# Kernel tuning notes

Hardware: AMD Instinct MI355X
Metric: run time of the kernel (lower is better)

The kernel has to match this reference:

```python
import jax, jax.numpy as jnp
import numpy as np

B, S, E = 4, 2048, 2048
NH, NKV, HD = 16, 4, 128  # num_heads, num_kv_heads, head_dim
GROUP = NH // NKV


def setup_inputs() -> dict:
    key = jax.random.key(0)
    ks = jax.random.split(key, 6)
    sc = 0.02
    return {
        "hidden_states": jax.random.normal(ks[0], (B, S, E), dtype=jnp.float32),
        "q_w": jax.random.normal(ks[1], (E, NH * HD), dtype=jnp.float32) * sc,
        "k_w": jax.random.normal(ks[2], (E, NKV * HD), dtype=jnp.float32) * sc,
        "v_w": jax.random.normal(ks[3], (E, NKV * HD), dtype=jnp.float32) * sc,
        "out_w": jax.random.normal(ks[4], (NH * HD, E), dtype=jnp.float32) * sc,
        "out_b": jnp.zeros((E,), dtype=jnp.float32),
    }


def reference(hidden_states, q_w, k_w, v_w, out_w, out_b):
    x = hidden_states
    # projections (no bias on q/k/v, bias on out_proj)
    q = (x @ q_w).reshape(B, S, NH, HD).transpose(0, 2, 1, 3)    # [B,NH,S,HD]
    k = (x @ k_w).reshape(B, S, NKV, HD).transpose(0, 2, 1, 3)   # [B,NKV,S,HD]
    v = (x @ v_w).reshape(B, S, NKV, HD).transpose(0, 2, 1, 3)   # [B,NKV,S,HD]

    # GQA: each kv head serves GROUP consecutive query heads (matches loop order)
    k_exp = jnp.repeat(k, GROUP, axis=1)  # [B,NH,S,HD]
    v_exp = jnp.repeat(v, GROUP, axis=1)

    # GPT-Neo: fp32 attention, NO 1/sqrt(d) scaling
    qf = q.astype(jnp.float32)
    kf = k_exp.astype(jnp.float32)
    scores = jnp.einsum("bhqd,bhkd->bhqk", qf, kf)  # [B,NH,S,S]

    causal = jnp.tril(jnp.ones((S, S), dtype=bool))[None, None]
    mask_value = jnp.finfo(scores.dtype).min
    scores = jnp.where(causal, scores, mask_value)

    attn = jax.nn.softmax(scores, axis=-1).astype(v.dtype)
    ctx = jnp.einsum("bhqk,bhkd->bhqd", attn, v_exp)  # [B,NH,S,HD]

    out = ctx.transpose(0, 2, 1, 3).reshape(B, S, NH * HD)
    return out @ out_w + out_b
```

## Files before the change

kernel.cpp:

```cpp
#include <hip/hip_runtime.h>

typedef unsigned short u16;
typedef unsigned int   u32;
typedef __attribute__((ext_vector_type(8))) _Float16 f16x8;
typedef __attribute__((ext_vector_type(2))) __fp16   fp16x2;
typedef __attribute__((ext_vector_type(4))) float    f32x4;

#define LOG2E 1.44269504088896340f

__device__ __forceinline__ u16 f2h(float x) {
  union { _Float16 h; u16 u; } c;
  c.h = (_Float16)x;
  return c.u;
}
__device__ __forceinline__ u32 pk2(float a, float b) {
  union { fp16x2 h; u32 u; } c;
  c.h = __builtin_amdgcn_cvt_pkrtz(a, b);
  return c.u;
}
__device__ __forceinline__ void swap32(u32& a, u32& b) {
  asm volatile("v_permlane32_swap_b32 %0, %1" : "+v"(a), "+v"(b));
}
__device__ __forceinline__ void swap16(u32& a, u32& b) {
  asm volatile("v_permlane16_swap_b32 %0, %1" : "+v"(a), "+v"(b));
}
__device__ __forceinline__ void gload16(const u16* g, u16* l) {
  __builtin_amdgcn_global_load_lds(
      (const __attribute__((address_space(1))) void*)g,
      (__attribute__((address_space(3))) void*)l, 16, 0, 0);
}
__device__ __forceinline__ f32x4 MFMA(f16x8 a, f16x8 b, f32x4 c) {
  return __builtin_amdgcn_mfma_f32_16x16x32_f16(a, b, c, 0, 0, 0);
}

__global__ void conv_f16(const float4* __restrict__ src, u16* __restrict__ d, int n4) {
  int i = blockIdx.x * 256 + threadIdx.x;
  if (i >= n4) return;
  float4 v = src[i];
  union { u16 u[4]; uint2 q; } H;
  H.u[0] = f2h(v.x); H.u[1] = f2h(v.y); H.u[2] = f2h(v.z); H.u[3] = f2h(v.w);
  *(uint2*)&d[(size_t)i * 4] = H.q;
}

__global__ void transpose_f16(const float* __restrict__ src, int K, int N,
                              u16* __restrict__ d, int rowOff) {
  __shared__ float t[32][33];
  int n0 = blockIdx.x * 32, k0 = blockIdx.y * 32;
  int tx = threadIdx.x, ty = threadIdx.y;
#pragma unroll
  for (int i = 0; i < 4; ++i)
    t[ty + 8 * i][tx] = src[(size_t)(k0 + ty + 8 * i) * N + n0 + tx];
  __syncthreads();
#pragma unroll
  for (int i = 0; i < 4; ++i) {
    int n = n0 + ty + 8 * i, k = k0 + tx;
    d[(size_t)(rowOff + n) * 2048 + k] = f2h(t[tx][ty + 8 * i]);
  }
}

__global__ __launch_bounds__(512) void gemm_qkv(
    const u16* __restrict__ A, const u16* __restrict__ B,
    u16* __restrict__ Qf, u16* __restrict__ Kf, u16* __restrict__ VT) {
  const int K = 2048;
  const int NS = K / 32;
  __shared__ u16 As[2][256 * 32];
  __shared__ u16 Bs[2][128 * 32];
  int tid = threadIdx.x;
  int l = tid & 63, w = tid >> 6;
  int lr = l & 15, lg = l >> 4;
  int wr = w >> 1, wc = w & 1;
  int p = blockIdx.x;
  int lidx = (p & 7) * 96 + (p >> 3);
  int bx = lidx % 24, by = lidx / 24;
  int rowA = by * 256, colB = bx * 128;
  int r0 = tid >> 2;
  int ssrc = (((tid & 3) ^ ((r0 >> 1) & 3))) * 8;
  const u16* ga = A + (size_t)(rowA + r0) * K + ssrc;
  const u16* gb = B + (size_t)(colB + r0) * K + ssrc;
  size_t half = (size_t)128 * K;
  f32x4 acc[4][4] = {};
  int swz = (lr >> 1) & 3;

  auto STAGE = [&](int kb, int bi) {
    gload16(ga + kb, &As[bi][tid * 8]);
    gload16(ga + kb + half, &As[bi][4096 + tid * 8]);
    gload16(gb + kb, &Bs[bi][tid * 8]);
  };
  auto COMPUTE = [&](int bi) {
    f16x8 ah[4], bh4[4];
#pragma unroll
    for (int i = 0; i < 4; ++i) {
      ah[i]  = *(const f16x8*)&As[bi][(wr * 64 + i * 16 + lr) * 32 + (lg ^ swz) * 8];
      bh4[i] = *(const f16x8*)&Bs[bi][(wc * 64 + i * 16 + lr) * 32 + (lg ^ swz) * 8];
    }
    __builtin_amdgcn_s_setprio(1);
#pragma unroll
    for (int i = 0; i < 4; ++i)
#pragma unroll
      for (int j = 0; j < 4; ++j)
        acc[i][j] = MFMA(ah[i], bh4[j], acc[i][j]);
    __builtin_amdgcn_s_setprio(0);
  };

  STAGE(0, 0);
  asm volatile("s_waitcnt vmcnt(0)" ::: "memory");
  __builtin_amdgcn_sched_barrier(0);
  __builtin_amdgcn_s_barrier();
  __builtin_amdgcn_sched_barrier(0);
  for (int t = 0; t < NS; ++t) {
    if (t + 1 < NS) STAGE((t + 1) * 32, (t + 1) & 1);
    COMPUTE(t & 1);
    asm volatile("s_waitcnt vmcnt(0) lgkmcnt(0)" ::: "memory");
    __builtin_amdgcn_sched_barrier(0);
    __builtin_amdgcn_s_barrier();
    __builtin_amdgcn_sched_barrier(0);
  }

#pragma unroll
  for (int i = 0; i < 4; ++i) {
    int row0 = rowA + wr * 64 + i * 16 + lg * 4;
#pragma unroll
    for (int j = 0; j < 4; ++j) {
      int c = colB + wc * 64 + j * 16 + lr;
      f32x4 v = acc[i][j];
      if (c < 2048) {
#pragma unroll
        for (int r = 0; r < 4; ++r)
          Qf[(size_t)(row0 + r) * 2048 + c] = f2h(v[r]);
      } else if (c < 2560) {
        int ck = c - 2048;
#pragma unroll
        for (int r = 0; r < 4; ++r)
          Kf[(size_t)(row0 + r) * 512 + ck] = f2h(v[r]);
      } else {
        int cv = c - 2560, kvh = cv >> 7, d = cv & 127;
        int b = row0 >> 11, t2 = row0 & 2047;
        union { u16 u[4]; uint2 q; } P;
#pragma unroll
        for (int r = 0; r < 4; ++r) P.u[r] = f2h(v[r]);
        *(uint2*)&VT[((size_t)(b * 4 + kvh) * 128 + d) * 2048 + t2] = P.q;
      }
    }
  }
}

__global__ __launch_bounds__(512) void gemm_out(
    const u16* __restrict__ A, const u16* __restrict__ B,
    float* __restrict__ Out, const float* __restrict__ bias) {
  const int K = 2048;
  const int NS = K / 32;
  __shared__ u16 As[2][256 * 32];
  __shared__ u16 Bs[2][128 * 32];
  int tid = threadIdx.x;
  int l = tid & 63, w = tid >> 6;
  int lr = l & 15, lg = l >> 4;
  int wr = w >> 1, wc = w & 1;
  int p = blockIdx.x;
  int lidx = (p & 7) * 64 + (p >> 3);
  int bx = lidx & 15, by = lidx >> 4;
  int rowA = by * 256, colB = bx * 128;
  int r0 = tid >> 2;
  int ssrc = (((tid & 3) ^ ((r0 >> 1) & 3))) * 8;
  const u16* ga = A + (size_t)(rowA + r0) * K + ssrc;
  const u16* gb = B + (size_t)(colB + r0) * K + ssrc;
  size_t half = (size_t)128 * K;
  f32x4 acc[4][4] = {};
  int swz = (lr >> 1) & 3;

  auto STAGE = [&](int kb, int bi) {
    gload16(ga + kb, &As[bi][tid * 8]);
    gload16(ga + kb + half, &As[bi][4096 + tid * 8]);
    gload16(gb + kb, &Bs[bi][tid * 8]);
  };
  auto COMPUTE = [&](int bi) {
    f16x8 ah[4], bh4[4];
#pragma unroll
    for (int i = 0; i < 4; ++i) {
      ah[i]  = *(const f16x8*)&As[bi][(wr * 64 + i * 16 + lr) * 32 + (lg ^ swz) * 8];
      bh4[i] = *(const f16x8*)&Bs[bi][(wc * 64 + i * 16 + lr) * 32 + (lg ^ swz) * 8];
    }
    __builtin_amdgcn_s_setprio(1);
#pragma unroll
    for (int i = 0; i < 4; ++i)
#pragma unroll
      for (int j = 0; j < 4; ++j)
        acc[i][j] = MFMA(ah[i], bh4[j], acc[i][j]);
    __builtin_amdgcn_s_setprio(0);
  };

  STAGE(0, 0);
  asm volatile("s_waitcnt vmcnt(0)" ::: "memory");
  __builtin_amdgcn_sched_barrier(0);
  __builtin_amdgcn_s_barrier();
  __builtin_amdgcn_sched_barrier(0);
  for (int t = 0; t < NS; ++t) {
    if (t + 1 < NS) STAGE((t + 1) * 32, (t + 1) & 1);
    COMPUTE(t & 1);
    asm volatile("s_waitcnt vmcnt(0) lgkmcnt(0)" ::: "memory");
    __builtin_amdgcn_sched_barrier(0);
    __builtin_amdgcn_s_barrier();
    __builtin_amdgcn_sched_barrier(0);
  }

#pragma unroll
  for (int i = 0; i < 4; ++i) {
    int row0 = rowA + wr * 64 + i * 16 + lg * 4;
#pragma unroll
    for (int j = 0; j < 4; ++j) {
      int c = colB + wc * 64 + j * 16 + lr;
      float bb = bias[c];
#pragma unroll
      for (int r = 0; r < 4; ++r)
        Out[(size_t)(row0 + r) * 2048 + c] = acc[i][j][r] + bb;
    }
  }
}

__global__ __launch_bounds__(512) void attn_kernel(
    const u16* __restrict__ Qf, const u16* __restrict__ Kf,
    const u16* __restrict__ VT, u16* __restrict__ Ch) {
  __shared__ u16 Ks[2][64 * 128];
  __shared__ u16 Vs[2][128 * 64];

  int tid = threadIdx.x;
  int w = tid >> 6, l = tid & 63;
  int lr = l & 15, lg = l >> 4;

  int p = blockIdx.x;
  int bid = (p & 7) * 64 + (p >> 3);
  int pair = bid & 7;
  int hg = (bid >> 3) & 3;
  int kvh = (bid >> 5) & 3;
  int b = bid >> 7;
  int h = kvh * 4 + hg;

  const u16* Kb = Kf + (size_t)(b * 2048) * 512 + kvh * 128;
  const u16* Vb = VT + (size_t)((b * 4 + kvh) * 128) * 2048;

  auto STAGE_K = [&](int t, int bufi) {
    int kv0 = t * 64;
#pragma unroll
    for (int pp = 0; pp < 2; ++pp) {
      int o16 = pp * 512 + tid;
      int krow = o16 >> 4;
      int kslot = ((o16 & 15) ^ (krow & 7)) * 8;
      gload16(Kb + (size_t)(kv0 + krow) * 512 + kslot, &Ks[bufi][o16 * 8]);
    }
  };
  auto STAGE_V = [&](int t, int bufi) {
    int kv0 = t * 64;
#pragma unroll
    for (int pp = 0; pp < 2; ++pp) {
      int o16 = pp * 512 + tid;
      int vrow = o16 >> 3;
      int vslot = ((o16 & 7) ^ (vrow & 7)) * 8;
      gload16(Vb + (size_t)vrow * 2048 + kv0 + vslot, &Vs[bufi][o16 * 8]);
    }
  };

  for (int pass = 0; pass < 2; ++pass) {
    int tIdx = pass == 0 ? (15 - pair) : pair;
    int q0 = tIdx * 128;
    int qr0 = q0 + w * 16;
    int nt = q0 / 64 + 2;

    size_t qbase = (size_t)(b * 2048 + qr0 + lr) * 2048 + h * 128 + lg * 8;
    f16x8 qf[4];
#pragma unroll
    for (int d = 0; d < 4; ++d)
      qf[d] = *(const f16x8*)(Qf + qbase + d * 32);

    f32x4 o[8] = {};
    float mrun = -3e38f;
    float lp = 0.f;

    STAGE_K(0, 0);
    STAGE_V(0, 0);
    asm volatile("s_waitcnt vmcnt(0)" ::: "memory");
    __builtin_amdgcn_sched_barrier(0);
    __builtin_amdgcn_s_barrier();
    __builtin_amdgcn_sched_barrier(0);

    int cur = 0;
    for (int t = 0; t < nt; ++t) {
      int kv0 = t * 64;
      bool more = (t + 1 < nt);
      if (more) {
        STAGE_K(t + 1, cur ^ 1);
        STAGE_V(t + 1, cur ^ 1);
      }
      bool compute = (kv0 <= qr0 + 15);

      if (compute) {
        f32x4 s[4] = {};
        __builtin_amdgcn_s_setprio(1);
#pragma unroll
        for (int d = 0; d < 4; ++d) {
#pragma unroll
          for (int n = 0; n < 4; ++n) {
            int row = n * 16 + lr;
            int sl = ((d * 4 + lg) ^ (row & 7)) * 8;
            f16x8 kf = *(const f16x8*)&Ks[cur][row * 128 + sl];
            s[n] = MFMA(kf, qf[d], s[n]);
          }
        }
        __builtin_amdgcn_s_setprio(0);
        if (kv0 + 63 > qr0) {
#pragma unroll
          for (int n = 0; n < 4; ++n)
#pragma unroll
            for (int r = 0; r < 4; ++r)
              if (kv0 + n * 16 + lg * 4 + r > qr0 + lr) s[n][r] = -3e38f;
        }
        float m0 = fmaxf(fmaxf(s[0][0], s[0][1]), fmaxf(s[0][2], s[0][3]));
        float m1 = fmaxf(fmaxf(s[1][0], s[1][1]), fmaxf(s[1][2], s[1][3]));
        float m2 = fmaxf(fmaxf(s[2][0], s[2][1]), fmaxf(s[2][2], s[2][3]));
        float m3 = fmaxf(fmaxf(s[3][0], s[3][1]), fmaxf(s[3][2], s[3][3]));
        float rowmax = fmaxf(fmaxf(m0, m1), fmaxf(m2, m3));
        if (__any(rowmax > mrun + 8.f)) {
          float tm = rowmax;
          tm = fmaxf(tm, __shfl_xor(tm, 16));
          tm = fmaxf(tm, __shfl_xor(tm, 32));
          float mn = fmaxf(mrun, tm);
          float alpha = __builtin_amdgcn_exp2f((mrun - mn) * LOG2E);
          mrun = mn;
          lp *= alpha;
#pragma unroll
          for (int dt = 0; dt < 8; ++dt)
#pragma unroll
            for (int r = 0; r < 4; ++r) o[dt][r] *= alpha;
        }
        float mL = mrun * LOG2E;
        float pv[4][4];
#pragma unroll
        for (int n = 0; n < 4; ++n)
#pragma unroll
          for (int r = 0; r < 4; ++r) {
            pv[n][r] = __builtin_amdgcn_exp2f(fmaf(s[n][r], LOG2E, -mL));
            lp += pv[n][r];
          }
        u32 A0[4], A1[4];
#pragma unroll
        for (int n = 0; n < 4; ++n) {
          A0[n] = pk2(pv[n][0], pv[n][1]);
          A1[n] = pk2(pv[n][2], pv[n][3]);
        }
        swap32(A0[0], A0[2]); swap32(A0[1], A0[3]);
        swap32(A1[0], A1[2]); swap32(A1[1], A1[3]);
        swap16(A0[0], A0[2]); swap16(A0[1], A0[3]);
        swap16(A1[0], A1[2]); swap16(A1[1], A1[3]);
        swap32(A0[0], A0[1]); swap32(A0[2], A0[3]);
        swap32(A1[0], A1[1]); swap32(A1[2], A1[3]);
        union { u32 w4[4]; f16x8 v; } P0, P1;
        P0.w4[0] = A0[0]; P0.w4[1] = A1[0]; P0.w4[2] = A0[2]; P0.w4[3] = A1[2];
        P1.w4[0] = A0[1]; P1.w4[1] = A1[1]; P1.w4[2] = A0[3]; P1.w4[3] = A1[3];
        __builtin_amdgcn_s_setprio(1);
#pragma unroll
        for (int n2 = 0; n2 < 2; ++n2) {
          f16x8 pf = n2 ? P1.v : P0.v;
#pragma unroll
          for (int dt = 0; dt < 8; ++dt) {
            int d = dt * 16 + lr;
            f16x8 vf = *(const f16x8*)&Vs[cur][d * 64 + (((n2 * 4 + lg) ^ (lr & 7)) * 8)];
            o[dt] = MFMA(vf, pf, o[dt]);
          }
        }
        __builtin_amdgcn_s_setprio(0);
      }
      asm volatile("s_waitcnt vmcnt(0) lgkmcnt(0)" ::: "memory");
      __builtin_amdgcn_sched_barrier(0);
      __builtin_amdgcn_s_barrier();
      __builtin_amdgcn_sched_barrier(0);
      cur ^= 1;
    }
    lp += __shfl_xor(lp, 16);
    lp += __shfl_xor(lp, 32);
    float inv = 1.0f / lp;
    size_t orow = (size_t)(b * 2048 + qr0 + lr) * 2048 + h * 128 + lg * 4;
#pragma unroll
    for (int dt = 0; dt < 8; ++dt) {
      uint2 pkt;
      pkt.x = pk2(o[dt][0] * inv, o[dt][1] * inv);
      pkt.y = pk2(o[dt][2] * inv, o[dt][3] * inv);
      *(uint2*)&Ch[orow + dt * 16] = pkt;
    }
  }
}

extern "C" void kernel_launch(void* const* d_in, const int* in_sizes, int n_in,
                              void* d_out, int out_size, void* d_ws, size_t ws_size,
                              hipStream_t stream) {
  const float* X  = (const float*)d_in[0];
  const float* qw = (const float*)d_in[1];
  const float* kw = (const float*)d_in[2];
  const float* vw = (const float*)d_in[3];
  const float* ow = (const float*)d_in[4];
  const float* ob = (const float*)d_in[5];
  float* Out = (float*)d_out;

  char* ws = (char*)d_ws;
  size_t off = 0;
  auto alloc = [&](size_t bytes) -> void* {
    void* p = ws + off;
    off += (bytes + 255) & ~(size_t)255;
    return p;
  };
  const size_t MK = (size_t)8192 * 2048;
  u16* Xf = (u16*)alloc(MK * 2);
  u16* Bt = (u16*)alloc((size_t)3072 * 2048 * 2);
  u16* OW = (u16*)alloc((size_t)2048 * 2048 * 2);
  u16* Qf = (u16*)alloc(MK * 2);
  u16* Kf = (u16*)alloc((size_t)8192 * 512 * 2);
  u16* VT = (u16*)alloc((size_t)8192 * 512 * 2);
  u16* Ch = (u16*)alloc(MK * 2);

  conv_f16<<<dim3(16384), dim3(256), 0, stream>>>((const float4*)X, Xf, (int)(MK / 4));
  dim3 tb(32, 8);
  transpose_f16<<<dim3(64, 64), tb, 0, stream>>>(qw, 2048, 2048, Bt, 0);
  transpose_f16<<<dim3(16, 64), tb, 0, stream>>>(kw, 2048, 512, Bt, 2048);
  transpose_f16<<<dim3(16, 64), tb, 0, stream>>>(vw, 2048, 512, Bt, 2560);
  transpose_f16<<<dim3(64, 64), tb, 0, stream>>>(ow, 2048, 2048, OW, 0);
  gemm_qkv<<<dim3(768), dim3(512), 0, stream>>>(Xf, Bt, Qf, Kf, VT);
  attn_kernel<<<dim3(512), dim3(512), 0, stream>>>(Qf, Kf, VT, Ch);
  gemm_out<<<dim3(512), dim3(512), 0, stream>>>(Ch, OW, Out, ob);
}
```

Measured before the change: 356.8 us.

## Triple-buffer GEMM smem with two-stage-ahead prefetch and split compute phases

Both projection GEMM kernels move from double to triple-buffered LDS, prefetching the K-slice two iterations ahead and waiting with partial vmcnt rather than draining all loads. Each iteration is split into two MFMA halves with a barrier between them, and the global loads are interleaved with the LDS reads so memory latency overlaps compute. The cost is 50% more shared memory per block, which may lower occupancy, plus an extra barrier per iteration.

```diff
diff --git a/kernel.cpp b/kernel.cpp
--- a/kernel.cpp
+++ b/kernel.cpp
@@ -63,8 +63,8 @@
     u16* __restrict__ Qf, u16* __restrict__ Kf, u16* __restrict__ VT) {
   const int K = 2048;
   const int NS = K / 32;
-  __shared__ u16 As[2][256 * 32];
-  __shared__ u16 Bs[2][128 * 32];
+  __shared__ u16 As[3][256 * 32];
+  __shared__ u16 Bs[3][128 * 32];
   int tid = threadIdx.x;
   int l = tid & 63, w = tid >> 6;
   int lr = l & 15, lg = l >> 4;
@@ -80,38 +80,62 @@
   size_t half = (size_t)128 * K;
   f32x4 acc[4][4] = {};
   int swz = (lr >> 1) & 3;
-
-  auto STAGE = [&](int kb, int bi) {
-    gload16(ga + kb, &As[bi][tid * 8]);
-    gload16(ga + kb + half, &As[bi][4096 + tid * 8]);
-    gload16(gb + kb, &Bs[bi][tid * 8]);
-  };
-  auto COMPUTE = [&](int bi) {
-    f16x8 ah[4], bh4[4];
-#pragma unroll
-    for (int i = 0; i < 4; ++i) {
-      ah[i]  = *(const f16x8*)&As[bi][(wr * 64 + i * 16 + lr) * 32 + (lg ^ swz) * 8];
-      bh4[i] = *(const f16x8*)&Bs[bi][(wc * 64 + i * 16 + lr) * 32 + (lg ^ swz) * 8];
-    }
-    __builtin_amdgcn_s_setprio(1);
-#pragma unroll
-    for (int i = 0; i < 4; ++i)
-#pragma unroll
-      for (int j = 0; j < 4; ++j)
-        acc[i][j] = MFMA(ah[i], bh4[j], acc[i][j]);
-    __builtin_amdgcn_s_setprio(0);
-  };
-
-  STAGE(0, 0);
-  asm volatile("s_waitcnt vmcnt(0)" ::: "memory");
+  int aoff = (wr * 64 + lr) * 32 + (lg ^ swz) * 8;
+  int boff = (wc * 64 + lr) * 32 + (lg ^ swz) * 8;
+
+  gload16(ga, &As[0][tid * 8]);
+  gload16(ga + half, &As[0][4096 + tid * 8]);
+  gload16(gb, &Bs[0][tid * 8]);
+  gload16(ga + 32, &As[1][tid * 8]);
+  gload16(ga + 32 + half, &As[1][4096 + tid * 8]);
+  gload16(gb + 32, &Bs[1][tid * 8]);
+  asm volatile("s_waitcnt vmcnt(3)" ::: "memory");
   __builtin_amdgcn_sched_barrier(0);
   __builtin_amdgcn_s_barrier();
   __builtin_amdgcn_sched_barrier(0);
+
   for (int t = 0; t < NS; ++t) {
-    if (t + 1 < NS) STAGE((t + 1) * 32, (t + 1) & 1);
-    COMPUTE(t & 1);
-    asm volatile("s_waitcnt vmcnt(0) lgkmcnt(0)" ::: "memory");
-    __builtin_amdgcn_sched_barrier(0);
+    int cur = t % 3, nxt = (t + 2) % 3;
+    bool pre = (t + 2 < NS);
+    int kb2 = (t + 2) * 32;
+    f16x8 ah[4], bh0, bh1;
+#pragma unroll
+    for (int i = 0; i < 4; ++i)
+      ah[i] = *(const f16x8*)&As[cur][aoff + i * 16 * 32];
+    bh0 = *(const f16x8*)&Bs[cur][boff];
+    bh1 = *(const f16x8*)&Bs[cur][boff + 16 * 32];
+    if (pre) {
+      gload16(ga + kb2, &As[nxt][tid * 8]);
+      gload16(ga + kb2 + half, &As[nxt][4096 + tid * 8]);
+    }
+    asm volatile("s_waitcnt lgkmcnt(0)" ::: "memory");
+    __builtin_amdgcn_sched_barrier(0);
+    __builtin_amdgcn_s_setprio(1);
+#pragma unroll
+    for (int i = 0; i < 4; ++i) {
+      acc[i][0] = MFMA(ah[i], bh0, acc[i][0]);
+      acc[i][1] = MFMA(ah[i], bh1, acc[i][1]);
+    }
+    __builtin_amdgcn_s_setprio(0);
+    __builtin_amdgcn_s_barrier();
+    __builtin_amdgcn_sched_barrier(0);
+    f16x8 bh2 = *(const f16x8*)&Bs[cur][boff + 32 * 32];
+    f16x8 bh3 = *(const f16x8*)&Bs[cur][boff + 48 * 32];
+    if (pre) gload16(gb + kb2, &Bs[nxt][tid * 8]);
+    if (pre) {
+      asm volatile("s_waitcnt vmcnt(3)" ::: "memory");
+    } else {
+      asm volatile("s_waitcnt vmcnt(0)" ::: "memory");
+    }
+    asm volatile("s_waitcnt lgkmcnt(0)" ::: "memory");
+    __builtin_amdgcn_sched_barrier(0);
+    __builtin_amdgcn_s_setprio(1);
+#pragma unroll
+    for (int i = 0; i < 4; ++i) {
+      acc[i][2] = MFMA(ah[i], bh2, acc[i][2]);
+      acc[i][3] = MFMA(ah[i], bh3, acc[i][3]);
+    }
+    __builtin_amdgcn_s_setprio(0);
     __builtin_amdgcn_s_barrier();
     __builtin_amdgcn_sched_barrier(0);
   }
@@ -149,8 +173,8 @@
     float* __restrict__ Out, const float* __restrict__ bias) {
   const int K = 2048;
   const int NS = K / 32;
-  __shared__ u16 As[2][256 * 32];
-  __shared__ u16 Bs[2][128 * 32];
+  __shared__ u16 As[3][256 * 32];
+  __shared__ u16 Bs[3][128 * 32];
   int tid = threadIdx.x;
   int l = tid & 63, w = tid >> 6;
   int lr = l & 15, lg = l >> 4;
@@ -166,38 +190,62 @@
   size_t half = (size_t)128 * K;
   f32x4 acc[4][4] = {};
   int swz = (lr >> 1) & 3;
-
-  auto STAGE = [&](int kb, int bi) {
-    gload16(ga + kb, &As[bi][tid * 8]);
-    gload16(ga + kb + half, &As[bi][4096 + tid * 8]);
-    gload16(gb + kb, &Bs[bi][tid * 8]);
-  };
-  auto COMPUTE = [&](int bi) {
-    f16x8 ah[4], bh4[4];
-#pragma unroll
-    for (int i = 0; i < 4; ++i) {
-      ah[i]  = *(const f16x8*)&As[bi][(wr * 64 + i * 16 + lr) * 32 + (lg ^ swz) * 8];
-      bh4[i] = *(const f16x8*)&Bs[bi][(wc * 64 + i * 16 + lr) * 32 + (lg ^ swz) * 8];
-    }
-    __builtin_amdgcn_s_setprio(1);
-#pragma unroll
-    for (int i = 0; i < 4; ++i)
-#pragma unroll
-      for (int j = 0; j < 4; ++j)
-        acc[i][j] = MFMA(ah[i], bh4[j], acc[i][j]);
-    __builtin_amdgcn_s_setprio(0);
-  };
-
-  STAGE(0, 0);
-  asm volatile("s_waitcnt vmcnt(0)" ::: "memory");
+  int aoff = (wr * 64 + lr) * 32 + (lg ^ swz) * 8;
+  int boff = (wc * 64 + lr) * 32 + (lg ^ swz) * 8;
+
+  gload16(ga, &As[0][tid * 8]);
+  gload16(ga + half, &As[0][4096 + tid * 8]);
+  gload16(gb, &Bs[0][tid * 8]);
+  gload16(ga + 32, &As[1][tid * 8]);
+  gload16(ga + 32 + half, &As[1][4096 + tid * 8]);
+  gload16(gb + 32, &Bs[1][tid * 8]);
+  asm volatile("s_waitcnt vmcnt(3)" ::: "memory");
   __builtin_amdgcn_sched_barrier(0);
   __builtin_amdgcn_s_barrier();
   __builtin_amdgcn_sched_barrier(0);
+
   for (int t = 0; t < NS; ++t) {
-    if (t + 1 < NS) STAGE((t + 1) * 32, (t + 1) & 1);
-    COMPUTE(t & 1);
-    asm volatile("s_waitcnt vmcnt(0) lgkmcnt(0)" ::: "memory");
-    __builtin_amdgcn_sched_barrier(0);
+    int cur = t % 3, nxt = (t + 2) % 3;
+    bool pre = (t + 2 < NS);
+    int kb2 = (t + 2) * 32;
+    f16x8 ah[4], bh0, bh1;
+#pragma unroll
+    for (int i = 0; i < 4; ++i)
+      ah[i] = *(const f16x8*)&As[cur][aoff + i * 16 * 32];
+    bh0 = *(const f16x8*)&Bs[cur][boff];
+    bh1 = *(const f16x8*)&Bs[cur][boff + 16 * 32];
+    if (pre) {
+      gload16(ga + kb2, &As[nxt][tid * 8]);
+      gload16(ga + kb2 + half, &As[nxt][4096 + tid * 8]);
+    }
+    asm volatile("s_waitcnt lgkmcnt(0)" ::: "memory");
+    __builtin_amdgcn_sched_barrier(0);
+    __builtin_amdgcn_s_setprio(1);
+#pragma unroll
+    for (int i = 0; i < 4; ++i) {
+      acc[i][0] = MFMA(ah[i], bh0, acc[i][0]);
+      acc[i][1] = MFMA(ah[i], bh1, acc[i][1]);
+    }
+    __builtin_amdgcn_s_setprio(0);
+    __builtin_amdgcn_s_barrier();
+    __builtin_amdgcn_sched_barrier(0);
+    f16x8 bh2 = *(const f16x8*)&Bs[cur][boff + 32 * 32];
+    f16x8 bh3 = *(const f16x8*)&Bs[cur][boff + 48 * 32];
+    if (pre) gload16(gb + kb2, &Bs[nxt][tid * 8]);
+    if (pre) {
+      asm volatile("s_waitcnt vmcnt(3)" ::: "memory");
+    } else {
+      asm volatile("s_waitcnt vmcnt(0)" ::: "memory");
+    }
+    asm volatile("s_waitcnt lgkmcnt(0)" ::: "memory");
+    __builtin_amdgcn_sched_barrier(0);
+    __builtin_amdgcn_s_setprio(1);
+#pragma unroll
+    for (int i = 0; i < 4; ++i) {
+      acc[i][2] = MFMA(ah[i], bh2, acc[i][2]);
+      acc[i][3] = MFMA(ah[i], bh3, acc[i][3]);
+    }
+    __builtin_amdgcn_s_setprio(0);
     __builtin_amdgcn_s_barrier();
     __builtin_amdgcn_sched_barrier(0);
   }
```

After: 336.5 us. -5.7%, faster.
